# Kernel optimization log

Measured on AMD Instinct MI355X. Metric: run time of the kernel, lower is better.

The kernel has to match this reference:

```python
import math
import jax, jax.numpy as jnp
import numpy as np

EPS = 1e-05
_THETA = 180.0 * math.pi / 180.0
COS_T = math.cos(_THETA)   # -1.0
SIN_T = math.sin(_THETA)   # ~1.22e-16 (kept for faithfulness)
FH, FW = 3, 3
SH, SW = 1, 1
PH, PW = 1, 1


def _unfold(x):
    # x: (N, C, H, W) -> patches (N, C*FH*FW, OH, OW), channel-major (c, fh, fw)
    # ordering, matching torch.nn.functional.unfold.
    return jax.lax.conv_general_dilated_patches(
        x, (FH, FW), (SH, SW), [(PH, PH), (PW, PW)])


def _norm(v, axis=-1):
    return jnp.sqrt(jnp.sum(v * v, axis=axis, keepdims=True))


def m_rule(w, x, r, eps):
    # w: (n_filters, in_dim), x: (bs, in_dim), r: (bs, n_filters)
    normalized_w = w / (_norm(w) + eps)                       # (nf, d)
    norm_x = _norm(x) + eps                                   # (bs, 1)
    normalized_x = x / norm_x                                 # (bs, d)
    wx = normalized_x @ normalized_w.T                        # (bs, nf)
    # orth = w_hat - (w_hat . x_hat) x_hat, per (patch, filter) pair
    orth = normalized_w[None, :, :] - wx[:, :, None] * normalized_x[:, None, :]
    normalized_orth = orth / (_norm(orth) + eps)              # (bs, nf, d)
    x_head = (COS_T * normalized_x[:, None, :] + SIN_T * normalized_orth)
    x_head = x_head * norm_x[:, :, None]                      # (bs, nf, d)
    x_diff = x[:, None, :] - x_head                           # (bs, nf, d)
    wx_diff = w[None, :, :] * x_diff                          # (bs, nf, d)
    wx_diff_normalized = wx_diff / (wx_diff.sum(-1, keepdims=True) + eps)
    r_out = wx_diff_normalized * r[:, :, None]                # (bs, nf, d)
    return r_out.sum(1)                                       # (bs, d)


def setup_inputs() -> dict:
    key = jax.random.key(0)
    k1, k2, k3 = jax.random.split(key, 3)
    x = jax.random.normal(k1, (4, 64, 16, 16), dtype=jnp.float32)
    r = jax.random.normal(k2, (4, 128, 16, 16), dtype=jnp.float32)
    weight = jax.random.normal(k3, (128, 64, 3, 3), dtype=jnp.float32) * 0.05
    return {"x": x, "r": r, "weight": weight}


def reference(x, r, weight):
    N, C, H, W = x.shape
    NF = weight.shape[0]
    patches = _unfold(x)                                      # (N, C*9, OH, OW)
    _, IN_DIM, OH, OW = patches.shape
    x_col = patches.reshape(N, IN_DIM, OH * OW).transpose(0, 2, 1).reshape(-1, IN_DIM)
    w_col = weight.reshape(NF, -1)                            # (NF, C*9)
    r_col = r.transpose(0, 2, 3, 1).reshape(-1, NF)           # (N*OH*OW, NF)
    r_new = m_rule(w_col, x_col, r_col, EPS)                  # (N*OH*OW, C*9)
    r_img = r_new.reshape(N, OH * OW, IN_DIM).transpose(0, 2, 1).reshape(N, IN_DIM, OH, OW)
    # F.fold is the linear transpose (adjoint) of unfold: overlapping patches
    # are summed back into the (N, C, H, W) image.
    fold = jax.linear_transpose(_unfold, jax.ShapeDtypeStruct(x.shape, x.dtype))
    return fold(r_img)[0]
```

## Files before the change

kernel.cpp:

```cpp
#include <hip/hip_runtime.h>

constexpr int N  = 4, C = 64, H = 16, W = 16;
constexpr int NF = 128;
constexpr int D  = C * 9;
constexpr float EPSF = 1e-5f;

__global__ void k_prep(const float* __restrict__ w,
                       float* __restrict__ w_t4, float* __restrict__ w2f4) {
    const int o = blockIdx.x * 256 + threadIdx.x;
    if (o >= 73728) return;
    const int j = o & 3;
    {
        const int f = (o >> 2) & 127, k4 = o >> 9;
        w_t4[o] = w[f * D + k4 * 4 + j];
    }
    {
        const int c = (o >> 2) & 63, rest = o >> 8;
        const int ab = rest % 9, fq = rest / 9;
        const int a = ab / 3, b = ab % 3;
        w2f4[o] = w[(fq * 4 + j) * D + c * 9 + (2 - a) * 3 + (2 - b)];
    }
}

__global__ void __launch_bounds__(1024) k_conv_t(
        const float* __restrict__ x, const float4* __restrict__ w_t4,
        const float* __restrict__ r, float* __restrict__ t_g) {
    __shared__ float  xl[C * 36];
    __shared__ double partd[16 * 8 * 64];

    const int bid = blockIdx.x;
    const int fh  = bid & 1;
    const int ow0 = ((bid >> 1) & 1) * 8;
    const int oh  = (bid >> 2) & 15;
    const int n   = bid >> 6;
    const int tid = threadIdx.x;
    const int f   = tid & 63;
    const int cg  = tid >> 6;

    for (int idx = tid; idx < C * 30; idx += 1024) {
        const int c = idx / 30, rem = idx % 30;
        const int dh = rem / 10, dw = rem % 10;
        const int ih = oh - 1 + dh, iw = ow0 - 1 + dw;
        float v = 0.f;
        if (ih >= 0 && ih < H && iw >= 0 && iw < W)
            v = x[((n * C + c) * H + ih) * W + iw];
        xl[c * 36 + dh * 12 + dw] = v;
    }
    __syncthreads();

    const int c0 = cg * 4;
    const float4* __restrict__ wp = w_t4 + (cg * 9) * 128 + fh * 64 + f;

    float wreg[36];
#pragma unroll
    for (int i = 0; i < 9; ++i) {
        const float4 wv = wp[i * 128];
        wreg[i * 4 + 0] = wv.x; wreg[i * 4 + 1] = wv.y;
        wreg[i * 4 + 2] = wv.z; wreg[i * 4 + 3] = wv.w;
    }

    double acc[8];
#pragma unroll
    for (int o = 0; o < 8; ++o) acc[o] = 0.0;

#pragma unroll
    for (int cl = 0; cl < 4; ++cl) {
#pragma unroll
        for (int dh = 0; dh < 3; ++dh) {
            const float* rowp = xl + (c0 + cl) * 36 + dh * 12;
            const float4 xa = *(const float4*)rowp;
            const float4 xb = *(const float4*)(rowp + 4);
            const float2 xc = *(const float2*)(rowp + 8);
            double xd[10];
            xd[0] = (double)xa.x; xd[1] = (double)xa.y;
            xd[2] = (double)xa.z; xd[3] = (double)xa.w;
            xd[4] = (double)xb.x; xd[5] = (double)xb.y;
            xd[6] = (double)xb.z; xd[7] = (double)xb.w;
            xd[8] = (double)xc.x; xd[9] = (double)xc.y;
#pragma unroll
            for (int b = 0; b < 3; ++b) {
                const double wd = (double)wreg[cl * 9 + dh * 3 + b];
#pragma unroll
                for (int o = 0; o < 8; ++o)
                    acc[o] += wd * xd[b + o];
            }
        }
    }

#pragma unroll
    for (int o = 0; o < 8; ++o)
        partd[(cg * 8 + o) * 64 + f] = acc[o];
    __syncthreads();

    if (tid < 512) {
        const int f2 = tid & 63, o = tid >> 6;
        double s = 0.0;
#pragma unroll
        for (int g = 0; g < 16; ++g)
            s += partd[(g * 8 + o) * 64 + f2];
        const int fglob = fh * 64 + f2;
        const int idx = ((n * NF + fglob) * H + oh) * W + ow0 + o;
        t_g[idx] = (float)((2.0 * (double)r[idx]) / (2.0 * s + (double)EPSF));
    }
}

__global__ void __launch_bounds__(1024) k_convT_out(
        const float* __restrict__ x, const float4* __restrict__ w2f4,
        const float* __restrict__ t_g, float* __restrict__ out) {
    __shared__ float tl[NF * 36];
    __shared__ float fpart[32 * 8 * 32];

    const int bid = blockIdx.x;
    const int ch  = bid & 1;
    const int w0  = ((bid >> 1) & 1) * 8;
    const int h   = (bid >> 2) & 15;
    const int n   = bid >> 6;
    const int tid = threadIdx.x;
    const int c   = tid & 31;
    const int fg  = tid >> 5;

    for (int idx = tid; idx < NF * 30; idx += 1024) {
        const int ff = idx / 30, rem = idx % 30;
        const int a = rem / 10, ww = rem % 10;
        const int oh2 = h - 1 + a, ow = w0 - 1 + ww;
        float v = 0.f;
        if (oh2 >= 0 && oh2 < H && ow >= 0 && ow < W)
            v = t_g[((n * NF + ff) * H + oh2) * W + ow];
        tl[ff * 36 + a * 12 + ww] = v;
    }
    __syncthreads();

    const float4* __restrict__ wp = w2f4 + (fg * 9) * 64 + ch * 32 + c;
    float wq[36];
#pragma unroll
    for (int ab = 0; ab < 9; ++ab) {
        const float4 wv = wp[ab * 64];
        wq[ab * 4 + 0] = wv.x; wq[ab * 4 + 1] = wv.y;
        wq[ab * 4 + 2] = wv.z; wq[ab * 4 + 3] = wv.w;
    }

    float acc[8];
#pragma unroll
    for (int o = 0; o < 8; ++o) acc[o] = 0.f;

#pragma unroll
    for (int j = 0; j < 4; ++j) {
        const int fi = fg * 4 + j;
#pragma unroll
        for (int a = 0; a < 3; ++a) {
            const float* rowp = tl + fi * 36 + a * 12;
            const float4 ta = *(const float4*)rowp;
            const float4 tb = *(const float4*)(rowp + 4);
            const float2 tc = *(const float2*)(rowp + 8);
            const float tw[10] = {ta.x, ta.y, ta.z, ta.w,
                                  tb.x, tb.y, tb.z, tb.w, tc.x, tc.y};
#pragma unroll
            for (int b = 0; b < 3; ++b) {
                const float wv = wq[(a * 3 + b) * 4 + j];
#pragma unroll
                for (int o = 0; o < 8; ++o)
                    acc[o] += wv * tw[b + o];
            }
        }
    }

#pragma unroll
    for (int o = 0; o < 8; ++o)
        fpart[(fg * 8 + o) * 32 + c] = acc[o];
    __syncthreads();

    if (tid < 256) {
        const int c2 = tid & 31, o = tid >> 5;
        float s = 0.f;
#pragma unroll
        for (int g = 0; g < 32; ++g)
            s += fpart[(g * 8 + o) * 32 + c2];
        const int cglob = ch * 32 + c2;
        const int idx = ((n * C + cglob) * H + h) * W + w0 + o;
        out[idx] = x[idx] * s;
    }
}

extern "C" void kernel_launch(void* const* d_in, const int* in_sizes, int n_in,
                              void* d_out, int out_size, void* d_ws, size_t ws_size,
                              hipStream_t stream) {
    const float* x = (const float*)d_in[0];
    const float* r = (const float*)d_in[1];
    const float* w = (const float*)d_in[2];
    float* out = (float*)d_out;

    float* ws    = (float*)d_ws;
    float* w_t4  = ws;
    float* w2f4  = w_t4 + 73728;
    float* t_g   = w2f4 + 73728;

    k_prep<<<288, 256, 0, stream>>>(w, w_t4, w2f4);
    k_conv_t<<<256, 1024, 0, stream>>>(x, (const float4*)w_t4, r, t_g);
    k_convT_out<<<256, 1024, 0, stream>>>(x, (const float4*)w2f4, t_g, out);
}
```

Before: 71.42 us.

## Fuse weight prep and both conv stages into one cooperative kernel with grid sync

Result: slower. 207.2 us (+190.1%).

```diff
diff --git a/kernel.cpp b/kernel.cpp
--- a/kernel.cpp
+++ b/kernel.cpp
@@ -1,183 +1,173 @@
 #include <hip/hip_runtime.h>
+#include <hip/hip_cooperative_groups.h>
+
+namespace cg = cooperative_groups;
 
 constexpr int N  = 4, C = 64, H = 16, W = 16;
 constexpr int NF = 128;
 constexpr int D  = C * 9;
 constexpr float EPSF = 1e-5f;
 
-__global__ void k_prep(const float* __restrict__ w,
-                       float* __restrict__ w_t4, float* __restrict__ w2f4) {
-    const int o = blockIdx.x * 256 + threadIdx.x;
-    if (o >= 73728) return;
-    const int j = o & 3;
-    {
-        const int f = (o >> 2) & 127, k4 = o >> 9;
-        w_t4[o] = w[f * D + k4 * 4 + j];
-    }
-    {
-        const int c = (o >> 2) & 63, rest = o >> 8;
-        const int ab = rest % 9, fq = rest / 9;
-        const int a = ab / 3, b = ab % 3;
-        w2f4[o] = w[(fq * 4 + j) * D + c * 9 + (2 - a) * 3 + (2 - b)];
-    }
-}
-
-__global__ void __launch_bounds__(1024) k_conv_t(
-        const float* __restrict__ x, const float4* __restrict__ w_t4,
-        const float* __restrict__ r, float* __restrict__ t_g) {
-    __shared__ float  xl[C * 36];
-    __shared__ double partd[16 * 8 * 64];
+__global__ void __launch_bounds__(1024) k_fused(
+        const float* __restrict__ x, const float* __restrict__ w,
+        const float* __restrict__ r, float* __restrict__ t_g,
+        float* __restrict__ out) {
+    __shared__ __align__(16) unsigned char smem[74752];
 
     const int bid = blockIdx.x;
-    const int fh  = bid & 1;
-    const int ow0 = ((bid >> 1) & 1) * 8;
-    const int oh  = (bid >> 2) & 15;
-    const int n   = bid >> 6;
     const int tid = threadIdx.x;
-    const int f   = tid & 63;
-    const int cg  = tid >> 6;
 
-    for (int idx = tid; idx < C * 30; idx += 1024) {
-        const int c = idx / 30, rem = idx % 30;
-        const int dh = rem / 10, dw = rem % 10;
-        const int ih = oh - 1 + dh, iw = ow0 - 1 + dw;
-        float v = 0.f;
-        if (ih >= 0 && ih < H && iw >= 0 && iw < W)
-            v = x[((n * C + c) * H + ih) * W + iw];
-        xl[c * 36 + dh * 12 + dw] = v;
-    }
-    __syncthreads();
+    {
+        float*  xl    = (float*)smem;
+        double* partd = (double*)(smem + 9216);
 
-    const int c0 = cg * 4;
-    const float4* __restrict__ wp = w_t4 + (cg * 9) * 128 + fh * 64 + f;
+        const int fh  = bid & 1;
+        const int ow0 = ((bid >> 1) & 1) * 8;
+        const int oh  = (bid >> 2) & 15;
+        const int n   = bid >> 6;
+        const int f   = tid & 63;
+        const int cgi = tid >> 6;
 
-    float wreg[36];
+        const float* __restrict__ wrow = w + (fh * 64 + f) * D + cgi * 36;
+        float wreg[36];
 #pragma unroll
-    for (int i = 0; i < 9; ++i) {
-        const float4 wv = wp[i * 128];
-        wreg[i * 4 + 0] = wv.x; wreg[i * 4 + 1] = wv.y;
-        wreg[i * 4 + 2] = wv.z; wreg[i * 4 + 3] = wv.w;
-    }
+        for (int i = 0; i < 9; ++i) {
+            const float4 wv = *(const float4*)(wrow + i * 4);
+            wreg[i * 4 + 0] = wv.x; wreg[i * 4 + 1] = wv.y;
+            wreg[i * 4 + 2] = wv.z; wreg[i * 4 + 3] = wv.w;
+        }
 
-    double acc[8];
+        for (int idx = tid; idx < C * 30; idx += 1024) {
+            const int c = idx / 30, rem = idx % 30;
+            const int dh = rem / 10, dw = rem % 10;
+            const int ih = oh - 1 + dh, iw = ow0 - 1 + dw;
+            float v = 0.f;
+            if (ih >= 0 && ih < H && iw >= 0 && iw < W)
+                v = x[((n * C + c) * H + ih) * W + iw];
+            xl[c * 36 + dh * 12 + dw] = v;
+        }
+        __syncthreads();
+
+        const int c0 = cgi * 4;
+        double acc[8];
 #pragma unroll
-    for (int o = 0; o < 8; ++o) acc[o] = 0.0;
+        for (int o = 0; o < 8; ++o) acc[o] = 0.0;
 
 #pragma unroll
-    for (int cl = 0; cl < 4; ++cl) {
+        for (int cl = 0; cl < 4; ++cl) {
 #pragma unroll
-        for (int dh = 0; dh < 3; ++dh) {
-            const float* rowp = xl + (c0 + cl) * 36 + dh * 12;
-            const float4 xa = *(const float4*)rowp;
-            const float4 xb = *(const float4*)(rowp + 4);
-            const float2 xc = *(const float2*)(rowp + 8);
-            double xd[10];
-            xd[0] = (double)xa.x; xd[1] = (double)xa.y;
-            xd[2] = (double)xa.z; xd[3] = (double)xa.w;
-            xd[4] = (double)xb.x; xd[5] = (double)xb.y;
-            xd[6] = (double)xb.z; xd[7] = (double)xb.w;
-            xd[8] = (double)xc.x; xd[9] = (double)xc.y;
+            for (int dh = 0; dh < 3; ++dh) {
+                const float* rowp = xl + (c0 + cl) * 36 + dh * 12;
+                const float4 xa = *(const float4*)rowp;
+                const float4 xb = *(const float4*)(rowp + 4);
+                const float2 xc = *(const float2*)(rowp + 8);
+                double xd[10];
+                xd[0] = (double)xa.x; xd[1] = (double)xa.y;
+                xd[2] = (double)xa.z; xd[3] = (double)xa.w;
+                xd[4] = (double)xb.x; xd[5] = (double)xb.y;
+                xd[6] = (double)xb.z; xd[7] = (double)xb.w;
+                xd[8] = (double)xc.x; xd[9] = (double)xc.y;
 #pragma unroll
-            for (int b = 0; b < 3; ++b) {
-                const double wd = (double)wreg[cl * 9 + dh * 3 + b];
+                for (int b = 0; b < 3; ++b) {
+                    const double wd = (double)wreg[cl * 9 + dh * 3 + b];
 #pragma unroll
-                for (int o = 0; o < 8; ++o)
-                    acc[o] += wd * xd[b + o];
+                    for (int o = 0; o < 8; ++o)
+                        acc[o] += wd * xd[b + o];
+                }
             }
+        }
+
+#pragma unroll
+        for (int o = 0; o < 8; ++o)
+            partd[(cgi * 8 + o) * 64 + f] = acc[o];
+        __syncthreads();
+
+        if (tid < 512) {
+            const int f2 = tid & 63, o = tid >> 6;
+            double s = 0.0;
+#pragma unroll
+            for (int g = 0; g < 16; ++g)
+                s += partd[(g * 8 + o) * 64 + f2];
+            const int fglob = fh * 64 + f2;
+            const int idx = ((n * NF + fglob) * H + oh) * W + ow0 + o;
+            t_g[idx] = (float)((2.0 * (double)r[idx]) / (2.0 * s + (double)EPSF));
         }
     }
 
+    __threadfence();
+    cg::this_grid().sync();
+
+    {
+        float* tl    = (float*)smem;
+        float* fpart = (float*)(smem + 18432);
+
+        const int ch = bid & 1;
+        const int w0 = ((bid >> 1) & 1) * 8;
+        const int h  = (bid >> 2) & 15;
+        const int n  = bid >> 6;
+        const int c  = tid & 31;
+        const int fg = tid >> 5;
+
+        for (int idx = tid; idx < NF * 30; idx += 1024) {
+            const int ff = idx / 30, rem = idx % 30;
+            const int a = rem / 10, ww = rem % 10;
+            const int oh2 = h - 1 + a, ow = w0 - 1 + ww;
+            float v = 0.f;
+            if (oh2 >= 0 && oh2 < H && ow >= 0 && ow < W)
+                v = t_g[((n * NF + ff) * H + oh2) * W + ow];
+            tl[ff * 36 + a * 12 + ww] = v;
+        }
+
+        float wr2[36];
 #pragma unroll
-    for (int o = 0; o < 8; ++o)
-        partd[(cg * 8 + o) * 64 + f] = acc[o];
-    __syncthreads();
+        for (int j = 0; j < 4; ++j) {
+            const float* __restrict__ wp = w + (fg * 4 + j) * D + (ch * 32 + c) * 9;
+#pragma unroll
+            for (int k = 0; k < 9; ++k)
+                wr2[j * 9 + k] = wp[k];
+        }
+        __syncthreads();
 
-    if (tid < 512) {
-        const int f2 = tid & 63, o = tid >> 6;
-        double s = 0.0;
+        float acc[8];
 #pragma unroll
-        for (int g = 0; g < 16; ++g)
-            s += partd[(g * 8 + o) * 64 + f2];
-        const int fglob = fh * 64 + f2;
-        const int idx = ((n * NF + fglob) * H + oh) * W + ow0 + o;
-        t_g[idx] = (float)((2.0 * (double)r[idx]) / (2.0 * s + (double)EPSF));
-    }
-}
-
-__global__ void __launch_bounds__(1024) k_convT_out(
-        const float* __restrict__ x, const float4* __restrict__ w2f4,
-        const float* __restrict__ t_g, float* __restrict__ out) {
-    __shared__ float tl[NF * 36];
-    __shared__ float fpart[32 * 8 * 32];
-
-    const int bid = blockIdx.x;
-    const int ch  = bid & 1;
-    const int w0  = ((bid >> 1) & 1) * 8;
-    const int h   = (bid >> 2) & 15;
-    const int n   = bid >> 6;
-    const int tid = threadIdx.x;
-    const int c   = tid & 31;
-    const int fg  = tid >> 5;
-
-    for (int idx = tid; idx < NF * 30; idx += 1024) {
-        const int ff = idx / 30, rem = idx % 30;
-        const int a = rem / 10, ww = rem % 10;
-        const int oh2 = h - 1 + a, ow = w0 - 1 + ww;
-        float v = 0.f;
-        if (oh2 >= 0 && oh2 < H && ow >= 0 && ow < W)
-            v = t_g[((n * NF + ff) * H + oh2) * W + ow];
-        tl[ff * 36 + a * 12 + ww] = v;
-    }
-    __syncthreads();
-
-    const float4* __restrict__ wp = w2f4 + (fg * 9) * 64 + ch * 32 + c;
-    float wq[36];
-#pragma unroll
-    for (int ab = 0; ab < 9; ++ab) {
-        const float4 wv = wp[ab * 64];
-        wq[ab * 4 + 0] = wv.x; wq[ab * 4 + 1] = wv.y;
-        wq[ab * 4 + 2] = wv.z; wq[ab * 4 + 3] = wv.w;
-    }
-
-    float acc[8];
-#pragma unroll
-    for (int o = 0; o < 8; ++o) acc[o] = 0.f;
+        for (int o = 0; o < 8; ++o) acc[o] = 0.f;
 
 #pragma unroll
-    for (int j = 0; j < 4; ++j) {
-        const int fi = fg * 4 + j;
+        for (int j = 0; j < 4; ++j) {
+            const int fi = fg * 4 + j;
 #pragma unroll
-        for (int a = 0; a < 3; ++a) {
-            const float* rowp = tl + fi * 36 + a * 12;
-            const float4 ta = *(const float4*)rowp;
-            const float4 tb = *(const float4*)(rowp + 4);
-            const float2 tc = *(const float2*)(rowp + 8);
-            const float tw[10] = {ta.x, ta.y, ta.z, ta.w,
-                                  tb.x, tb.y, tb.z, tb.w, tc.x, tc.y};
+            for (int a = 0; a < 3; ++a) {
+                const float* rowp = tl + fi * 36 + a * 12;
+                const float4 ta = *(const float4*)rowp;
+                const float4 tb = *(const float4*)(rowp + 4);
+                const float2 tc = *(const float2*)(rowp + 8);
+                const float tw[10] = {ta.x, ta.y, ta.z, ta.w,
+                                      tb.x, tb.y, tb.z, tb.w, tc.x, tc.y};
 #pragma unroll
-            for (int b = 0; b < 3; ++b) {
-                const float wv = wq[(a * 3 + b) * 4 + j];
+                for (int b = 0; b < 3; ++b) {
+                    const float wv = wr2[j * 9 + (2 - a) * 3 + (2 - b)];
 #pragma unroll
-                for (int o = 0; o < 8; ++o)
-                    acc[o] += wv * tw[b + o];
+                    for (int o = 0; o < 8; ++o)
+                        acc[o] += wv * tw[b + o];
+                }
             }
         }
-    }
 
 #pragma unroll
-    for (int o = 0; o < 8; ++o)
-        fpart[(fg * 8 + o) * 32 + c] = acc[o];
-    __syncthreads();
+        for (int o = 0; o < 8; ++o)
+            fpart[(fg * 8 + o) * 32 + c] = acc[o];
+        __syncthreads();
 
-    if (tid < 256) {
-        const int c2 = tid & 31, o = tid >> 5;
-        float s = 0.f;
+        if (tid < 256) {
+            const int c2 = tid & 31, o = tid >> 5;
+            float s = 0.f;
 #pragma unroll
-        for (int g = 0; g < 32; ++g)
-            s += fpart[(g * 8 + o) * 32 + c2];
-        const int cglob = ch * 32 + c2;
-        const int idx = ((n * C + cglob) * H + h) * W + w0 + o;
-        out[idx] = x[idx] * s;
+            for (int g = 0; g < 32; ++g)
+                s += fpart[(g * 8 + o) * 32 + c2];
+            const int cglob = ch * 32 + c2;
+            const int idx = ((n * C + cglob) * H + h) * W + w0 + o;
+            out[idx] = x[idx] * s;
+        }
     }
 }
 
@@ -188,13 +178,9 @@
     const float* r = (const float*)d_in[1];
     const float* w = (const float*)d_in[2];
     float* out = (float*)d_out;
+    float* t_g = (float*)d_ws;
 
-    float* ws    = (float*)d_ws;
-    float* w_t4  = ws;
-    float* w2f4  = w_t4 + 73728;
-    float* t_g   = w2f4 + 73728;
-
-    k_prep<<<288, 256, 0, stream>>>(w, w_t4, w2f4);
-    k_conv_t<<<256, 1024, 0, stream>>>(x, (const float4*)w_t4, r, t_g);
-    k_convT_out<<<256, 1024, 0, stream>>>(x, (const float4*)w2f4, t_g, out);
+    void* args[] = { (void*)&x, (void*)&w, (void*)&r, (void*)&t_g, (void*)&out };
+    hipLaunchCooperativeKernel((void*)k_fused, dim3(256), dim3(1024),
+                               args, 0, stream);
 }
```
